# Kernel tuning notes

Measured on AMD Instinct MI355X. Metric: run time of the kernel, lower is better.

Reference implementation:

```python
import jax, jax.numpy as jnp
import numpy as np

SD = 4          # spixel_downsize
EPS = 1e-5      # BatchNorm eps
SLOPE = 0.01    # nn.LeakyReLU() default negative_slope


def deconv3d(x, w, stride, pad):
    # w is in torch ConvTranspose3d layout: (in_ch, out_ch, kd, kh, kw).
    # Transposed conv == conv with lhs_dilation=stride, flipped kernel,
    # padding (k-1-p) per spatial dim.
    kd, kh, kw = w.shape[2], w.shape[3], w.shape[4]
    wc = jnp.transpose(jnp.flip(w, axis=(2, 3, 4)), (1, 0, 2, 3, 4))  # OIDHW
    pads = [(kd - 1 - pad[0],) * 2, (kh - 1 - pad[1],) * 2, (kw - 1 - pad[2],) * 2]
    return jax.lax.conv_general_dilated(
        x, wc, window_strides=(1, 1, 1), padding=pads,
        lhs_dilation=(stride, stride, stride),
        dimension_numbers=('NCDHW', 'OIDHW', 'NCDHW'))


def bn_lrelu(x, g, b, relu=True):
    # inference BatchNorm3d with running_mean=0, running_var=1 (fresh BN)
    scale = (g / jnp.sqrt(1.0 + EPS)).reshape(1, -1, 1, 1, 1)
    y = x * scale + b.reshape(1, -1, 1, 1, 1)
    return jax.nn.leaky_relu(y, SLOPE) if relu else y


def _sl(s):
    # shift s in {+1, 0, -1} -> (agg slice, cost slice) along one spatial dim
    if s == 1:
        return slice(SD, None), slice(None, -SD)
    if s == 0:
        return slice(None), slice(None)
    return slice(None, -SD), slice(SD, None)


def setup_inputs() -> dict:
    key = jax.random.key(0)
    ks = jax.random.split(key, 8)
    b, d, h, w = 1, 24, 64, 128
    f32 = jnp.float32
    cv1 = jax.random.normal(ks[0], (b, 32, d, h, w), f32)                 # cv[-1]
    cv0 = jax.random.normal(ks[1], (b, 16, 2 * d, 2 * h, 2 * w), f32)     # cv[-2]
    sp = jax.random.uniform(ks[2], (b, 9, 4 * h, 4 * w), f32)             # superpixel probs
    w0a = jax.random.normal(ks[3], (32, 32, 3, 1, 1), f32) * 0.05
    w0b = jax.random.normal(ks[4], (32, 16, 4, 2, 2), f32) * 0.05
    w1a = jax.random.normal(ks[5], (32, 16, 3, 1, 1), f32) * 0.05
    w1b = jax.random.normal(ks[6], (16, 1, 4, 2, 2), f32) * 0.05
    g0, g1, g2, g3 = (jnp.ones((c,), f32) for c in (32, 16, 16, 1))
    b0, b1, b2, b3 = (jnp.zeros((c,), f32) for c in (32, 16, 16, 1))
    return dict(cv1=cv1, cv0=cv0, sp=sp, w0a=w0a, w0b=w0b, w1a=w1a, w1b=w1b,
                g0=g0, g1=g1, g2=g2, g3=g3, b0=b0, b1=b1, b2=b2, b3=b3)


def reference(cv1, cv0, sp, w0a, w0b, w1a, w1b, g0, g1, g2, g3, b0, b1, b2, b3):
    # conv[0]: BasicConv(32->32, k(3,1,1), s1, p(1,0,0)) + BasicConv(32->16, k(4,2,2), s2, p(1,0,0))
    x = bn_lrelu(deconv3d(cv1, w0a, 1, (1, 0, 0)), g0, b0)
    x = bn_lrelu(deconv3d(x, w0b, 2, (1, 0, 0)), g1, b1)
    x = jnp.concatenate((x, cv0), axis=1)
    # conv[1] (sp==2 branch): 32->16 then 16->out_dim, bn=relu=bnrelu=True
    x = bn_lrelu(deconv3d(x, w1a, 1, (1, 0, 0)), g2, b2)
    cost = bn_lrelu(deconv3d(x, w1b, 2, (1, 0, 0)), g3, b3)  # (b, 1, 4d, 4h, 4w)

    sp5 = sp[:, None]  # (b, 1, 9, H, W)
    agg = jnp.zeros_like(cost)
    k = 0
    for hy in (1, 0, -1):        # 9 fixed superpixel-neighbor shifts
        ah, ch = _sl(hy)
        for wx in (1, 0, -1):
            aw, cw = _sl(wx)
            wgt = sp5[:, :, k, ah, aw][:, :, None]  # (b,1,1,H',W')
            agg = agg.at[:, :, :, ah, aw].add(cost[:, :, :, ch, cw] * wgt)
            k += 1
    return agg
```

## Files before the change

kernel.cpp:

```cpp
#include <hip/hip_runtime.h>
#include <hip/hip_bf16.h>

typedef __hip_bfloat16 bf16;

constexpr int cD0 = 24,  cH0 = 64,  cW0 = 128;
constexpr int cD1 = 48,  cH1 = 128, cW1 = 256;
constexpr int cD2 = 96,  cH2 = 256, cW2 = 512;
constexpr size_t PL0 = (size_t)cD0 * cH0 * cW0;
constexpr size_t PL1 = (size_t)cD1 * cH1 * cW1;
constexpr size_t PL2 = (size_t)cD2 * cH2 * cW2;

__device__ __forceinline__ float b2f(bf16 v) { return __bfloat162float(v); }
__device__ __forceinline__ bf16  f2b(float v) { return __float2bfloat16(v); }
__device__ __forceinline__ float lrelu(float v) { return v >= 0.f ? v : 0.01f * v; }

__global__ __launch_bounds__(256) void kA(const float* __restrict__ cv1,
                                          const float* __restrict__ w0a,
                                          const float* __restrict__ g0,
                                          const float* __restrict__ b0,
                                          bf16* __restrict__ x1) {
    __shared__ float lw[3][32][32];
    __shared__ float lsc[32], lbi[32];
    const int tid = threadIdx.x;
    for (int i = tid; i < 32 * 32 * 3; i += 256) {
        int ci = i / 96, r = i - ci * 96, co = r / 3, u = r - co * 3;
        lw[u][ci][co] = w0a[i];
    }
    if (tid < 32) {
        lsc[tid] = g0[tid] * (1.0f / sqrtf(1.0f + 1e-5f));
        lbi[tid] = b0[tid];
    }
    __syncthreads();

    const int pos = blockIdx.x * 256 + tid;
    const int x = pos & (cW0 - 1);
    const int y = (pos >> 7) & (cH0 - 1);
    const int z = pos >> 13;

    float acc[32];
    #pragma unroll
    for (int co = 0; co < 32; ++co) acc[co] = 0.f;

    #pragma unroll
    for (int u = 0; u < 3; ++u) {
        const int zi = z + 1 - u;
        if (zi < 0 || zi >= cD0) continue;
        const float* src = cv1 + (size_t)(zi * cH0 + y) * cW0 + x;
        for (int ci = 0; ci < 32; ++ci) {
            const float v = src[ci * PL0];
            const float4* wp = (const float4*)&lw[u][ci][0];
            #pragma unroll
            for (int q = 0; q < 8; ++q) {
                float4 wv = wp[q];
                acc[4*q+0] += v * wv.x; acc[4*q+1] += v * wv.y;
                acc[4*q+2] += v * wv.z; acc[4*q+3] += v * wv.w;
            }
        }
    }
    #pragma unroll
    for (int co = 0; co < 32; ++co)
        x1[co * PL0 + (size_t)(z * cH0 + y) * cW0 + x] =
            f2b(lrelu(acc[co] * lsc[co] + lbi[co]));
}

__global__ __launch_bounds__(256) void kB(const bf16* __restrict__ x1,
                                          const float* __restrict__ w0b,
                                          const float* __restrict__ g1,
                                          const float* __restrict__ b1,
                                          bf16* __restrict__ x2) {
    __shared__ float lw[4][2][32][2][16];
    __shared__ float lsc[16], lbi[16];
    const int tid = threadIdx.x;
    for (int i = tid; i < 8192; i += 256) {
        int ci = i >> 8, co = (i >> 4) & 15, kd = (i >> 2) & 3, kh = (i >> 1) & 1, kw = i & 1;
        lw[kd][kh][ci][kw][co] = w0b[i];
    }
    if (tid < 16) {
        lsc[tid] = g1[tid] * (1.0f / sqrtf(1.0f + 1e-5f));
        lbi[tid] = b1[tid];
    }
    __syncthreads();

    const int t    = blockIdx.x * 256 + tid;
    const int lane = t & 63;
    const int row  = t >> 6;
    const int oh = row & 127, od = row >> 7;
    const int ih = oh >> 1, kh = oh & 1;
    const int kw = lane & 1;
    const int p  = (od + 1) & 1;
    const int iwb = lane >> 1;

    float acc[4][16];
    #pragma unroll
    for (int k = 0; k < 4; ++k)
        #pragma unroll
        for (int co = 0; co < 16; ++co) acc[k][co] = 0.f;

    #pragma unroll
    for (int j = 0; j < 2; ++j) {
        const int kd = p + 2 * j;
        const int id = (od + 1 - kd) >> 1;
        if (id < 0 || id >= cD0) continue;
        const bf16* src = x1 + (size_t)(id * cH0 + ih) * cW0 + iwb;
        for (int ci = 0; ci < 32; ++ci) {
            const float v0 = b2f(src[ci * PL0 +  0]);
            const float v1 = b2f(src[ci * PL0 + 32]);
            const float v2 = b2f(src[ci * PL0 + 64]);
            const float v3 = b2f(src[ci * PL0 + 96]);
            const float4* wp = (const float4*)&lw[kd][kh][ci][kw][0];
            #pragma unroll
            for (int q = 0; q < 4; ++q) {
                float4 wv = wp[q];
                acc[0][4*q+0] += v0 * wv.x; acc[0][4*q+1] += v0 * wv.y;
                acc[0][4*q+2] += v0 * wv.z; acc[0][4*q+3] += v0 * wv.w;
                acc[1][4*q+0] += v1 * wv.x; acc[1][4*q+1] += v1 * wv.y;
                acc[1][4*q+2] += v1 * wv.z; acc[1][4*q+3] += v1 * wv.w;
                acc[2][4*q+0] += v2 * wv.x; acc[2][4*q+1] += v2 * wv.y;
                acc[2][4*q+2] += v2 * wv.z; acc[2][4*q+3] += v2 * wv.w;
                acc[3][4*q+0] += v3 * wv.x; acc[3][4*q+1] += v3 * wv.y;
                acc[3][4*q+2] += v3 * wv.z; acc[3][4*q+3] += v3 * wv.w;
            }
        }
    }
    const size_t obase = (size_t)(od * cH1 + oh) * cW1 + lane;
    #pragma unroll
    for (int k = 0; k < 4; ++k)
        #pragma unroll
        for (int co = 0; co < 16; ++co)
            x2[co * PL1 + obase + 64 * k] =
                f2b(lrelu(acc[k][co] * lsc[co] + lbi[co]));
}

__global__ __launch_bounds__(256) void kD(const bf16* __restrict__ x2,
                                          const float* __restrict__ cv0,
                                          const float* __restrict__ w1a,
                                          const float* __restrict__ g2,
                                          const float* __restrict__ b2v,
                                          bf16* __restrict__ x3) {
    __shared__ float lw[3][32][16];
    __shared__ float lsc[16], lbi[16];
    const int tid = threadIdx.x;
    for (int i = tid; i < 1536; i += 256) {
        int ci = i / 48, r = i - ci * 48, co = r / 3, u = r - co * 3;
        lw[u][ci][co] = w1a[i];
    }
    if (tid < 16) {
        lsc[tid] = g2[tid] * (1.0f / sqrtf(1.0f + 1e-5f));
        lbi[tid] = b2v[tid];
    }
    __syncthreads();

    const int t    = blockIdx.x * 256 + tid;
    const int lane = t & 63;
    const int row  = t >> 6;
    const int y = row & 127, z = row >> 7;

    float acc[4][16];
    #pragma unroll
    for (int k = 0; k < 4; ++k)
        #pragma unroll
        for (int co = 0; co < 16; ++co) acc[k][co] = 0.f;

    #pragma unroll
    for (int u = 0; u < 3; ++u) {
        const int zi = z + 1 - u;
        if (zi < 0 || zi >= cD1) continue;
        const size_t base = (size_t)(zi * cH1 + y) * cW1 + lane;
        for (int ci = 0; ci < 16; ++ci) {
            const float v0 = b2f(x2[ci * PL1 + base +   0]);
            const float v1 = b2f(x2[ci * PL1 + base +  64]);
            const float v2 = b2f(x2[ci * PL1 + base + 128]);
            const float v3 = b2f(x2[ci * PL1 + base + 192]);
            const float4* wp = (const float4*)&lw[u][ci][0];
            #pragma unroll
            for (int q = 0; q < 4; ++q) {
                float4 wv = wp[q];
                acc[0][4*q+0] += v0 * wv.x; acc[0][4*q+1] += v0 * wv.y;
                acc[0][4*q+2] += v0 * wv.z; acc[0][4*q+3] += v0 * wv.w;
                acc[1][4*q+0] += v1 * wv.x; acc[1][4*q+1] += v1 * wv.y;
                acc[1][4*q+2] += v1 * wv.z; acc[1][4*q+3] += v1 * wv.w;
                acc[2][4*q+0] += v2 * wv.x; acc[2][4*q+1] += v2 * wv.y;
                acc[2][4*q+2] += v2 * wv.z; acc[2][4*q+3] += v2 * wv.w;
                acc[3][4*q+0] += v3 * wv.x; acc[3][4*q+1] += v3 * wv.y;
                acc[3][4*q+2] += v3 * wv.z; acc[3][4*q+3] += v3 * wv.w;
            }
        }
        for (int ci = 0; ci < 16; ++ci) {
            const float v0 = cv0[ci * PL1 + base +   0];
            const float v1 = cv0[ci * PL1 + base +  64];
            const float v2 = cv0[ci * PL1 + base + 128];
            const float v3 = cv0[ci * PL1 + base + 192];
            const float4* wp = (const float4*)&lw[u][16 + ci][0];
            #pragma unroll
            for (int q = 0; q < 4; ++q) {
                float4 wv = wp[q];
                acc[0][4*q+0] += v0 * wv.x; acc[0][4*q+1] += v0 * wv.y;
                acc[0][4*q+2] += v0 * wv.z; acc[0][4*q+3] += v0 * wv.w;
                acc[1][4*q+0] += v1 * wv.x; acc[1][4*q+1] += v1 * wv.y;
                acc[1][4*q+2] += v1 * wv.z; acc[1][4*q+3] += v1 * wv.w;
                acc[2][4*q+0] += v2 * wv.x; acc[2][4*q+1] += v2 * wv.y;
                acc[2][4*q+2] += v2 * wv.z; acc[2][4*q+3] += v2 * wv.w;
                acc[3][4*q+0] += v3 * wv.x; acc[3][4*q+1] += v3 * wv.y;
                acc[3][4*q+2] += v3 * wv.z; acc[3][4*q+3] += v3 * wv.w;
            }
        }
    }
    const size_t obase = (size_t)(z * cH1 + y) * cW1 + lane;
    #pragma unroll
    for (int k = 0; k < 4; ++k)
        #pragma unroll
        for (int co = 0; co < 16; ++co)
            x3[co * PL1 + obase + 64 * k] =
                f2b(lrelu(acc[k][co] * lsc[co] + lbi[co]));
}

__global__ __launch_bounds__(256) void kE(const bf16* __restrict__ x3,
                                          const float* __restrict__ w1b,
                                          const float* __restrict__ g3,
                                          const float* __restrict__ b3v,
                                          bf16* __restrict__ cost) {
    __shared__ float lw[256];
    const int tid = threadIdx.x;
    lw[tid] = w1b[tid];
    __syncthreads();

    const int t    = blockIdx.x * 256 + tid;
    const int lane = t & 63;
    const int rowq = t >> 6;
    const int iw = lane + 64 * (rowq & 3);
    const int ih = (rowq >> 2) & 127;
    const int od = rowq >> 9;
    const int p  = (od + 1) & 1;

    float a00 = 0.f, a01 = 0.f, a10 = 0.f, a11 = 0.f;
    #pragma unroll
    for (int j = 0; j < 2; ++j) {
        const int kd = p + 2 * j;
        const int id = (od + 1 - kd) >> 1;
        if (id < 0 || id >= cD1) continue;
        const size_t base = (size_t)(id * cH1 + ih) * cW1 + iw;
        #pragma unroll
        for (int ci = 0; ci < 16; ++ci) {
            const float v = b2f(x3[ci * PL1 + base]);
            const float* w = &lw[ci * 16 + kd * 4];
            a00 += v * w[0]; a01 += v * w[1];
            a10 += v * w[2]; a11 += v * w[3];
        }
    }
    const float sc = g3[0] * (1.0f / sqrtf(1.0f + 1e-5f));
    const float bi = b3v[0];
    union { uint u; ushort s[2]; } pk;
    const size_t ob = (size_t)(od * cH2 + 2 * ih) * cW2 + 2 * iw;
    pk.s[0] = __bfloat16_as_ushort(f2b(lrelu(a00 * sc + bi)));
    pk.s[1] = __bfloat16_as_ushort(f2b(lrelu(a01 * sc + bi)));
    *(uint*)(cost + ob) = pk.u;
    pk.s[0] = __bfloat16_as_ushort(f2b(lrelu(a10 * sc + bi)));
    pk.s[1] = __bfloat16_as_ushort(f2b(lrelu(a11 * sc + bi)));
    *(uint*)(cost + ob + cW2) = pk.u;
}

__global__ __launch_bounds__(256) void kF(const bf16* __restrict__ cost,
                                          const float* __restrict__ sp,
                                          float* __restrict__ out) {
    const int t    = blockIdx.x * 256 + threadIdx.x;
    const int lane = t & 63;
    const int rowq = t >> 6;
    const int x  = lane + 64 * (rowq & 7);
    const int y  = (rowq >> 3) & 255;
    const int d0 = (rowq >> 11) * 4;
    const size_t plane = (size_t)cH2 * cW2;

    float w[9];
    int cyc[3], cxc[3];
    #pragma unroll
    for (int r = 0; r < 3; ++r) {
        const int cy = y - 4 * (1 - r);
        const bool vy = (cy >= 0) && (cy < cH2);
        cyc[r] = vy ? cy : 0;
        #pragma unroll
        for (int c = 0; c < 3; ++c) {
            const int cx = x - 4 * (1 - c);
            const bool vx = (cx >= 0) && (cx < cW2);
            if (c == 0 || r == 0) {}
            w[r*3+c] = (vy && vx) ? sp[(size_t)(r*3+c) * plane + (size_t)y * cW2 + x] : 0.f;
            if (r == 0) cxc[c] = vx ? cx : 0;
        }
    }
    #pragma unroll
    for (int dd = 0; dd < 4; ++dd) {
        const int d = d0 + dd;
        const bf16* cp = cost + (size_t)d * plane;
        float acc = 0.f;
        #pragma unroll
        for (int r = 0; r < 3; ++r)
            #pragma unroll
            for (int c = 0; c < 3; ++c)
                acc += w[r*3+c] * b2f(cp[(size_t)cyc[r] * cW2 + cxc[c]]);
        out[(size_t)d * plane + (size_t)y * cW2 + x] = acc;
    }
}

extern "C" void kernel_launch(void* const* d_in, const int* in_sizes, int n_in,
                              void* d_out, int out_size, void* d_ws, size_t ws_size,
                              hipStream_t stream) {
    const float* cv1 = (const float*)d_in[0];
    const float* cv0 = (const float*)d_in[1];
    const float* sp  = (const float*)d_in[2];
    const float* w0a = (const float*)d_in[3];
    const float* w0b = (const float*)d_in[4];
    const float* w1a = (const float*)d_in[5];
    const float* w1b = (const float*)d_in[6];
    const float* g0  = (const float*)d_in[7];
    const float* g1  = (const float*)d_in[8];
    const float* g2  = (const float*)d_in[9];
    const float* g3  = (const float*)d_in[10];
    const float* b0  = (const float*)d_in[11];
    const float* b1  = (const float*)d_in[12];
    const float* b2  = (const float*)d_in[13];
    const float* b3  = (const float*)d_in[14];

    char* ws = (char*)d_ws;
    bf16* x1   = (bf16*)(ws);
    bf16* x2   = (bf16*)(ws + 12582912);
    bf16* x3   = (bf16*)(ws + 62914560);
    bf16* cost = (bf16*)(ws);

    kA<<<768,   256, 0, stream>>>(cv1, w0a, g0, b0, x1);
    kB<<<1536,  256, 0, stream>>>(x1, w0b, g1, b1, x2);
    kD<<<1536,  256, 0, stream>>>(x2, cv0, w1a, g2, b2, x3);
    kE<<<12288, 256, 0, stream>>>(x3, w1b, g3, b3, cost);
    kF<<<12288, 256, 0, stream>>>(cost, sp, (float*)d_out);
}
```

Measured before the change: 389.5 us.

## Vectorize loads and stores across kB, kD, kE, kF with contiguous per-thread pixels

Remaps thread-to-pixel assignment in four kernels so each thread owns adjacent output columns instead of columns strided by 64. Loads and stores of bf16 and fp32 tensors become packed uint, ushort4 or float4 accesses, and grid sizes for kE and kF are halved and quartered to match. This aims to cut memory instruction count and improve per-thread access width on these bandwidth-bound stages. In exchange, each wavefront now spans a wider address range per instruction, and kF's float4 loads of the superpixel map depend on alignment of the shifted offsets.

```diff
diff --git a/kernel.cpp b/kernel.cpp
--- a/kernel.cpp
+++ b/kernel.cpp
@@ -13,6 +13,8 @@
 __device__ __forceinline__ float b2f(bf16 v) { return __bfloat162float(v); }
 __device__ __forceinline__ bf16  f2b(float v) { return __float2bfloat16(v); }
 __device__ __forceinline__ float lrelu(float v) { return v >= 0.f ? v : 0.01f * v; }
+__device__ __forceinline__ float us2f(ushort u) { return __uint_as_float(((uint)u) << 16); }
+__device__ __forceinline__ ushort f2us(float v) { return __bfloat16_as_ushort(f2b(v)); }
 
 __global__ __launch_bounds__(256) void kA(const float* __restrict__ cv1,
                                           const float* __restrict__ w0a,
@@ -86,9 +88,8 @@
     const int row  = t >> 6;
     const int oh = row & 127, od = row >> 7;
     const int ih = oh >> 1, kh = oh & 1;
-    const int kw = lane & 1;
     const int p  = (od + 1) & 1;
-    const int iwb = lane >> 1;
+    const int iw0 = 2 * lane;
 
     float acc[4][16];
     #pragma unroll
@@ -101,34 +102,38 @@
         const int kd = p + 2 * j;
         const int id = (od + 1 - kd) >> 1;
         if (id < 0 || id >= cD0) continue;
-        const bf16* src = x1 + (size_t)(id * cH0 + ih) * cW0 + iwb;
+        const bf16* src = x1 + (size_t)(id * cH0 + ih) * cW0 + iw0;
+        #pragma unroll 4
         for (int ci = 0; ci < 32; ++ci) {
-            const float v0 = b2f(src[ci * PL0 +  0]);
-            const float v1 = b2f(src[ci * PL0 + 32]);
-            const float v2 = b2f(src[ci * PL0 + 64]);
-            const float v3 = b2f(src[ci * PL0 + 96]);
-            const float4* wp = (const float4*)&lw[kd][kh][ci][kw][0];
+            const uint pk = *(const uint*)(src + ci * PL0);
+            const float v0 = us2f((ushort)(pk & 0xffffu));
+            const float v1 = us2f((ushort)(pk >> 16));
+            const float4* wp0 = (const float4*)&lw[kd][kh][ci][0][0];
+            const float4* wp1 = (const float4*)&lw[kd][kh][ci][1][0];
             #pragma unroll
             for (int q = 0; q < 4; ++q) {
-                float4 wv = wp[q];
-                acc[0][4*q+0] += v0 * wv.x; acc[0][4*q+1] += v0 * wv.y;
-                acc[0][4*q+2] += v0 * wv.z; acc[0][4*q+3] += v0 * wv.w;
-                acc[1][4*q+0] += v1 * wv.x; acc[1][4*q+1] += v1 * wv.y;
-                acc[1][4*q+2] += v1 * wv.z; acc[1][4*q+3] += v1 * wv.w;
-                acc[2][4*q+0] += v2 * wv.x; acc[2][4*q+1] += v2 * wv.y;
-                acc[2][4*q+2] += v2 * wv.z; acc[2][4*q+3] += v2 * wv.w;
-                acc[3][4*q+0] += v3 * wv.x; acc[3][4*q+1] += v3 * wv.y;
-                acc[3][4*q+2] += v3 * wv.z; acc[3][4*q+3] += v3 * wv.w;
-            }
-        }
-    }
-    const size_t obase = (size_t)(od * cH1 + oh) * cW1 + lane;
-    #pragma unroll
-    for (int k = 0; k < 4; ++k)
-        #pragma unroll
-        for (int co = 0; co < 16; ++co)
-            x2[co * PL1 + obase + 64 * k] =
-                f2b(lrelu(acc[k][co] * lsc[co] + lbi[co]));
+                float4 w0 = wp0[q], w1 = wp1[q];
+                acc[0][4*q+0] += v0 * w0.x; acc[0][4*q+1] += v0 * w0.y;
+                acc[0][4*q+2] += v0 * w0.z; acc[0][4*q+3] += v0 * w0.w;
+                acc[1][4*q+0] += v0 * w1.x; acc[1][4*q+1] += v0 * w1.y;
+                acc[1][4*q+2] += v0 * w1.z; acc[1][4*q+3] += v0 * w1.w;
+                acc[2][4*q+0] += v1 * w0.x; acc[2][4*q+1] += v1 * w0.y;
+                acc[2][4*q+2] += v1 * w0.z; acc[2][4*q+3] += v1 * w0.w;
+                acc[3][4*q+0] += v1 * w1.x; acc[3][4*q+1] += v1 * w1.y;
+                acc[3][4*q+2] += v1 * w1.z; acc[3][4*q+3] += v1 * w1.w;
+            }
+        }
+    }
+    const size_t obase = (size_t)(od * cH1 + oh) * cW1 + 4 * lane;
+    #pragma unroll
+    for (int co = 0; co < 16; ++co) {
+        ushort4 s;
+        s.x = f2us(lrelu(acc[0][co] * lsc[co] + lbi[co]));
+        s.y = f2us(lrelu(acc[1][co] * lsc[co] + lbi[co]));
+        s.z = f2us(lrelu(acc[2][co] * lsc[co] + lbi[co]));
+        s.w = f2us(lrelu(acc[3][co] * lsc[co] + lbi[co]));
+        *(ushort4*)(x2 + co * PL1 + obase) = s;
+    }
 }
 
 __global__ __launch_bounds__(256) void kD(const bf16* __restrict__ x2,
@@ -154,6 +159,7 @@
     const int lane = t & 63;
     const int row  = t >> 6;
     const int y = row & 127, z = row >> 7;
+    const int x0 = 4 * lane;
 
     float acc[4][16];
     #pragma unroll
@@ -165,12 +171,12 @@
     for (int u = 0; u < 3; ++u) {
         const int zi = z + 1 - u;
         if (zi < 0 || zi >= cD1) continue;
-        const size_t base = (size_t)(zi * cH1 + y) * cW1 + lane;
+        const size_t base = (size_t)(zi * cH1 + y) * cW1 + x0;
+        #pragma unroll 4
         for (int ci = 0; ci < 16; ++ci) {
-            const float v0 = b2f(x2[ci * PL1 + base +   0]);
-            const float v1 = b2f(x2[ci * PL1 + base +  64]);
-            const float v2 = b2f(x2[ci * PL1 + base + 128]);
-            const float v3 = b2f(x2[ci * PL1 + base + 192]);
+            const ushort4 pv = *(const ushort4*)(x2 + ci * PL1 + base);
+            const float v0 = us2f(pv.x), v1 = us2f(pv.y);
+            const float v2 = us2f(pv.z), v3 = us2f(pv.w);
             const float4* wp = (const float4*)&lw[u][ci][0];
             #pragma unroll
             for (int q = 0; q < 4; ++q) {
@@ -185,11 +191,10 @@
                 acc[3][4*q+2] += v3 * wv.z; acc[3][4*q+3] += v3 * wv.w;
             }
         }
+        #pragma unroll 4
         for (int ci = 0; ci < 16; ++ci) {
-            const float v0 = cv0[ci * PL1 + base +   0];
-            const float v1 = cv0[ci * PL1 + base +  64];
-            const float v2 = cv0[ci * PL1 + base + 128];
-            const float v3 = cv0[ci * PL1 + base + 192];
+            const float4 fv = *(const float4*)(cv0 + ci * PL1 + base);
+            const float v0 = fv.x, v1 = fv.y, v2 = fv.z, v3 = fv.w;
             const float4* wp = (const float4*)&lw[u][16 + ci][0];
             #pragma unroll
             for (int q = 0; q < 4; ++q) {
@@ -205,13 +210,16 @@
             }
         }
     }
-    const size_t obase = (size_t)(z * cH1 + y) * cW1 + lane;
-    #pragma unroll
-    for (int k = 0; k < 4; ++k)
-        #pragma unroll
-        for (int co = 0; co < 16; ++co)
-            x3[co * PL1 + obase + 64 * k] =
-                f2b(lrelu(acc[k][co] * lsc[co] + lbi[co]));
+    const size_t obase = (size_t)(z * cH1 + y) * cW1 + x0;
+    #pragma unroll
+    for (int co = 0; co < 16; ++co) {
+        ushort4 s;
+        s.x = f2us(lrelu(acc[0][co] * lsc[co] + lbi[co]));
+        s.y = f2us(lrelu(acc[1][co] * lsc[co] + lbi[co]));
+        s.z = f2us(lrelu(acc[2][co] * lsc[co] + lbi[co]));
+        s.w = f2us(lrelu(acc[3][co] * lsc[co] + lbi[co]));
+        *(ushort4*)(x3 + co * PL1 + obase) = s;
+    }
 }
 
 __global__ __launch_bounds__(256) void kE(const bf16* __restrict__ x3,
@@ -227,36 +235,45 @@
     const int t    = blockIdx.x * 256 + tid;
     const int lane = t & 63;
     const int rowq = t >> 6;
-    const int iw = lane + 64 * (rowq & 3);
-    const int ih = (rowq >> 2) & 127;
-    const int od = rowq >> 9;
-    const int p  = (od + 1) & 1;
-
-    float a00 = 0.f, a01 = 0.f, a10 = 0.f, a11 = 0.f;
+    const int iwp = lane + 64 * (rowq & 1);
+    const int ih  = (rowq >> 1) & 127;
+    const int od  = rowq >> 8;
+    const int p   = (od + 1) & 1;
+    const int iw0 = 2 * iwp;
+
+    float a[2][2][2] = {};
     #pragma unroll
     for (int j = 0; j < 2; ++j) {
         const int kd = p + 2 * j;
         const int id = (od + 1 - kd) >> 1;
         if (id < 0 || id >= cD1) continue;
-        const size_t base = (size_t)(id * cH1 + ih) * cW1 + iw;
+        const size_t base = (size_t)(id * cH1 + ih) * cW1 + iw0;
         #pragma unroll
         for (int ci = 0; ci < 16; ++ci) {
-            const float v = b2f(x3[ci * PL1 + base]);
+            const uint pk = *(const uint*)(x3 + ci * PL1 + base);
+            const float v0 = us2f((ushort)(pk & 0xffffu));
+            const float v1 = us2f((ushort)(pk >> 16));
             const float* w = &lw[ci * 16 + kd * 4];
-            a00 += v * w[0]; a01 += v * w[1];
-            a10 += v * w[2]; a11 += v * w[3];
+            a[0][0][0] += v0 * w[0]; a[0][0][1] += v0 * w[1];
+            a[0][1][0] += v0 * w[2]; a[0][1][1] += v0 * w[3];
+            a[1][0][0] += v1 * w[0]; a[1][0][1] += v1 * w[1];
+            a[1][1][0] += v1 * w[2]; a[1][1][1] += v1 * w[3];
         }
     }
     const float sc = g3[0] * (1.0f / sqrtf(1.0f + 1e-5f));
     const float bi = b3v[0];
-    union { uint u; ushort s[2]; } pk;
-    const size_t ob = (size_t)(od * cH2 + 2 * ih) * cW2 + 2 * iw;
-    pk.s[0] = __bfloat16_as_ushort(f2b(lrelu(a00 * sc + bi)));
-    pk.s[1] = __bfloat16_as_ushort(f2b(lrelu(a01 * sc + bi)));
-    *(uint*)(cost + ob) = pk.u;
-    pk.s[0] = __bfloat16_as_ushort(f2b(lrelu(a10 * sc + bi)));
-    pk.s[1] = __bfloat16_as_ushort(f2b(lrelu(a11 * sc + bi)));
-    *(uint*)(cost + ob + cW2) = pk.u;
+    const size_t ob = (size_t)(od * cH2 + 2 * ih) * cW2 + 4 * iwp;
+    ushort4 s;
+    s.x = f2us(lrelu(a[0][0][0] * sc + bi));
+    s.y = f2us(lrelu(a[0][0][1] * sc + bi));
+    s.z = f2us(lrelu(a[1][0][0] * sc + bi));
+    s.w = f2us(lrelu(a[1][0][1] * sc + bi));
+    *(ushort4*)(cost + ob) = s;
+    s.x = f2us(lrelu(a[0][1][0] * sc + bi));
+    s.y = f2us(lrelu(a[0][1][1] * sc + bi));
+    s.z = f2us(lrelu(a[1][1][0] * sc + bi));
+    s.w = f2us(lrelu(a[1][1][1] * sc + bi));
+    *(ushort4*)(cost + ob + cW2) = s;
 }
 
 __global__ __launch_bounds__(256) void kF(const bf16* __restrict__ cost,
@@ -265,12 +282,12 @@
     const int t    = blockIdx.x * 256 + threadIdx.x;
     const int lane = t & 63;
     const int rowq = t >> 6;
-    const int x  = lane + 64 * (rowq & 7);
-    const int y  = (rowq >> 3) & 255;
-    const int d0 = (rowq >> 11) * 4;
+    const int x0 = 4 * (lane + 64 * (rowq & 1));
+    const int y  = (rowq >> 1) & 255;
+    const int d0 = (rowq >> 9) * 4;
     const size_t plane = (size_t)cH2 * cW2;
 
-    float w[9];
+    float4 wq[9];
     int cyc[3], cxc[3];
     #pragma unroll
     for (int r = 0; r < 3; ++r) {
@@ -279,24 +296,33 @@
         cyc[r] = vy ? cy : 0;
         #pragma unroll
         for (int c = 0; c < 3; ++c) {
-            const int cx = x - 4 * (1 - c);
+            const int cx = x0 - 4 * (1 - c);
             const bool vx = (cx >= 0) && (cx < cW2);
-            if (c == 0 || r == 0) {}
-            w[r*3+c] = (vy && vx) ? sp[(size_t)(r*3+c) * plane + (size_t)y * cW2 + x] : 0.f;
             if (r == 0) cxc[c] = vx ? cx : 0;
+            if (vy && vx)
+                wq[r*3+c] = *(const float4*)(sp + (size_t)(r*3+c) * plane + (size_t)y * cW2 + x0);
+            else
+                wq[r*3+c] = make_float4(0.f, 0.f, 0.f, 0.f);
         }
     }
     #pragma unroll
     for (int dd = 0; dd < 4; ++dd) {
         const int d = d0 + dd;
         const bf16* cp = cost + (size_t)d * plane;
-        float acc = 0.f;
-        #pragma unroll
-        for (int r = 0; r < 3; ++r)
-            #pragma unroll
-            for (int c = 0; c < 3; ++c)
-                acc += w[r*3+c] * b2f(cp[(size_t)cyc[r] * cW2 + cxc[c]]);
-        out[(size_t)d * plane + (size_t)y * cW2 + x] = acc;
+        float ax = 0.f, ay = 0.f, az = 0.f, aw = 0.f;
+        #pragma unroll
+        for (int r = 0; r < 3; ++r) {
+            const bf16* rp = cp + (size_t)cyc[r] * cW2;
+            #pragma unroll
+            for (int c = 0; c < 3; ++c) {
+                const ushort4 u = *(const ushort4*)(rp + cxc[c]);
+                const float4 w = wq[r*3+c];
+                ax += w.x * us2f(u.x); ay += w.y * us2f(u.y);
+                az += w.z * us2f(u.z); aw += w.w * us2f(u.w);
+            }
+        }
+        float4 o; o.x = ax; o.y = ay; o.z = az; o.w = aw;
+        *(float4*)(out + (size_t)d * plane + (size_t)y * cW2 + x0) = o;
     }
 }
 
@@ -325,9 +351,9 @@
     bf16* x3   = (bf16*)(ws + 62914560);
     bf16* cost = (bf16*)(ws);
 
-    kA<<<768,   256, 0, stream>>>(cv1, w0a, g0, b0, x1);
-    kB<<<1536,  256, 0, stream>>>(x1, w0b, g1, b1, x2);
-    kD<<<1536,  256, 0, stream>>>(x2, cv0, w1a, g2, b2, x3);
-    kE<<<12288, 256, 0, stream>>>(x3, w1b, g3, b3, cost);
-    kF<<<12288, 256, 0, stream>>>(cost, sp, (float*)d_out);
-}
+    kA<<<768,  256, 0, stream>>>(cv1, w0a, g0, b0, x1);
+    kB<<<1536, 256, 0, stream>>>(x1, w0b, g1, b1, x2);
+    kD<<<1536, 256, 0, stream>>>(x2, cv0, w1a, g2, b2, x3);
+    kE<<<6144, 256, 0, stream>>>(x3, w1b, g3, b3, cost);
+    kF<<<3072, 256, 0, stream>>>(cost, sp, (float*)d_out);
+}
```

Measured after the change: 402.9 us. 1.03x slower.
